# Optimization experiments

Measured on AMD Instinct MI355X. Metric: run time of the kernel, lower is better.

Reference implementation:

```python
import jax, jax.numpy as jnp
import numpy as np

T, B, I, H, L = 512, 128, 512, 512, 2


def setup_inputs() -> dict:
    key = jax.random.key(0)
    ks = jax.random.split(key, 9)
    s = 1.0 / np.sqrt(H)  # torch LSTM init: U(-1/sqrt(H), 1/sqrt(H))
    u = lambda k, shape: jax.random.uniform(k, shape, jnp.float32, -s, s)
    return {
        "input_seq": jax.random.normal(ks[0], (T, B, I), jnp.float32),
        "W_ih0": u(ks[1], (4 * H, I)),
        "W_hh0": u(ks[2], (4 * H, H)),
        "b_ih0": u(ks[3], (4 * H,)),
        "b_hh0": u(ks[4], (4 * H,)),
        "W_ih1": u(ks[5], (4 * H, H)),
        "W_hh1": u(ks[6], (4 * H, H)),
        "b_ih1": u(ks[7], (4 * H,)),
        "b_hh1": u(ks[8], (4 * H,)),
    }


def _lstm_layer(x, W_ih, W_hh, b_ih, b_hh):
    # x: (T, B, in). Gate order matches torch: i, f, g, o.
    Bv = x.shape[1]
    Hv = W_hh.shape[1]
    # Precompute input projections for all timesteps (one big GEMM).
    x_proj = jnp.einsum('tbi,gi->tbg', x, W_ih) + b_ih + b_hh  # (T,B,4H)

    def step(carry, xp):
        h, c = carry
        gates = xp + h @ W_hh.T  # (B,4H)
        i, f, g, o = jnp.split(gates, 4, axis=-1)
        c = jax.nn.sigmoid(f) * c + jax.nn.sigmoid(i) * jnp.tanh(g)
        h = jax.nn.sigmoid(o) * jnp.tanh(c)
        return (h, c), h

    h0 = jnp.zeros((Bv, Hv), x.dtype)
    _, hs = jax.lax.scan(step, (h0, h0), x_proj)
    return hs  # (T,B,H)


def reference(input_seq, W_ih0, W_hh0, b_ih0, b_hh0, W_ih1, W_hh1, b_ih1, b_hh1):
    h1 = _lstm_layer(input_seq, W_ih0, W_hh0, b_ih0, b_hh0)
    h2 = _lstm_layer(h1, W_ih1, W_hh1, b_ih1, b_hh1)
    return h2[-1]  # last timestep of top layer, (B,H)
```

## Files before the change

kernel.cpp:

```cpp
#include <hip/hip_runtime.h>

typedef _Float16 f16;
typedef _Float16 f16x8 __attribute__((ext_vector_type(8)));
typedef float    f32x16 __attribute__((ext_vector_type(16)));

#define T_STEPS 512
#define RING    16


__device__ __forceinline__ void gload_lds16(const void* g, void* l) {
  __builtin_amdgcn_global_load_lds((const __attribute__((address_space(1))) void*)g,
                                   (__attribute__((address_space(3))) void*)l,
                                   16, 0, 0);
}

__device__ __forceinline__ float sigm(float x) { return 1.0f / (1.0f + __expf(-x)); }
__device__ __forceinline__ float tanh_f(float x) { return 2.0f / (1.0f + __expf(-2.0f * x)) - 1.0f; }

__device__ __forceinline__ bool spin_until(int* p, int target) {
  int it = 0;
  while (__hip_atomic_load(p, __ATOMIC_RELAXED, __HIP_MEMORY_SCOPE_AGENT) < target) {
    __builtin_amdgcn_s_sleep(1);
    if (++it > (1 << 20)) return false;
  }
  return true;
}


__global__ void cvt_kernel(const float* __restrict__ in, f16* __restrict__ out, int n8) {
  int i = blockIdx.x * blockDim.x + threadIdx.x;
  if (i >= n8) return;
  const float4* p = (const float4*)in + (size_t)i * 2;
  float4 a = p[0], b = p[1];
  f16x8 v = {(f16)a.x, (f16)a.y, (f16)a.z, (f16)a.w,
             (f16)b.x, (f16)b.y, (f16)b.z, (f16)b.w};
  *((f16x8*)out + i) = v;
}


__launch_bounds__(256, 1)
__global__ void lstm_scan(const f16* __restrict__ X16,
                          f16* __restrict__ h1ring, f16* __restrict__ h2ring,
                          int* __restrict__ cnt1, int* __restrict__ cnt2,
                          const float* __restrict__ Wih0, const float* __restrict__ Whh0,
                          const float* __restrict__ bih0, const float* __restrict__ bhh0,
                          const float* __restrict__ Wih1, const float* __restrict__ Whh1,
                          const float* __restrict__ bih1, const float* __restrict__ bhh1,
                          float* __restrict__ out) {
  __shared__ __align__(16) char A_lds[65536];
  __shared__ float P[2][32][32];
  __shared__ float G[2][32][32];
  __shared__ float bias_lds[64];
  __shared__ float c_lds[512];

  const int bid  = blockIdx.x;
  const int xcd  = bid & 7;
  const int layer = xcd & 1;
  const int g    = xcd >> 1;
  const int j    = bid >> 3;
  const int tid  = threadIdx.x;
  const int w    = tid >> 6;
  const int lane = tid & 63;
  const int c32  = lane & 31;
  const int kgrp = lane >> 5;
  const int nt   = w & 1;
  const int kh   = w >> 1;

  const float* Wsrc = layer ? (kh ? Whh1 : Wih1) : (kh ? Whh0 : Wih0);
  const int q    = nt * 2 + (c32 >> 4);
  const int wcol = q * 512 + j * 16 + (c32 & 15);
  f16x8 wreg[32];
  {
    const float* wrow = Wsrc + (size_t)wcol * 512 + kgrp * 8;
#pragma unroll
    for (int s = 0; s < 32; ++s) {
      const float* p = wrow + s * 16;
      float4 a = *(const float4*)p;
      float4 b = *(const float4*)(p + 4);
      f16x8 v = {(f16)a.x, (f16)a.y, (f16)a.z, (f16)a.w,
                 (f16)b.x, (f16)b.y, (f16)b.z, (f16)b.w};
      wreg[s] = v;
    }
  }
  if (tid < 64) {
    int c = tid & 31, n = tid >> 5;
    int qq  = n * 2 + (c >> 4);
    int col = qq * 512 + j * 16 + (c & 15);
    bias_lds[tid] = layer ? (bih1[col] + bhh1[col]) : (bih0[col] + bhh0[col]);
  }
  for (int e = tid; e < 512; e += 256) c_lds[e] = 0.0f;
  __syncthreads();

  int* cntOwn = layer ? cnt2 : cnt1;
  const int b_stage = g * 32 + c32;

  bool alive = true;
  for (int t = 0; t < T_STEPS; ++t) {
    if (layer == 0 && w < 2) {
      const f16* base = X16 + (size_t)t * 65536;
      const f16* lsrc = base + (size_t)b_stage * 512 + nt * 256 + kgrp * 8;
      char* ldst = A_lds + w * 16384;
#pragma unroll
      for (int si = 0; si < 16; ++si) gload_lds16(lsrc + si * 16, ldst + si * 1024);
    }

    if (tid == 0) {
      if (alive) {
        if (layer == 0) {
          if (t > 0)     alive &= spin_until(&cnt1[(t - 1) * 4 + g], 32);
          if (t >= RING) alive &= spin_until(&cnt2[(t - RING) * 4 + g], 32);
        } else {
          alive &= spin_until(&cnt1[t * 4 + g], 32);
          if (t > 0) alive &= spin_until(&cnt2[(t - 1) * 4 + g], 32);
        }
      }
      __builtin_amdgcn_fence(__ATOMIC_ACQUIRE, "agent");
    }
    __syncthreads();

    {
      const f16* base = nullptr;
      if (layer == 0) {
        if (w >= 2) base = h1ring + (size_t)(t & (RING - 1)) * 65536;
      } else {
        base = (w < 2) ? (h1ring + (size_t)((t + 1) & (RING - 1)) * 65536)
                       : (h2ring + (size_t)(t & (RING - 1)) * 65536);
      }
      if (base) {
        const f16* lsrc = base + (size_t)b_stage * 512 + nt * 256 + kgrp * 8;
        char* ldst = A_lds + w * 16384;
#pragma unroll
        for (int si = 0; si < 16; ++si) gload_lds16(lsrc + si * 16, ldst + si * 1024);
      }
    }
    __syncthreads();

    f32x16 acc0 = {}, acc1 = {}, acc2 = {}, acc3 = {};
    {
      const char* afb = A_lds + kh * 32768 + kgrp * 512 + c32 * 16;
#pragma unroll
      for (int s = 0; s < 32; s += 4) {
        f16x8 a0 = *(const f16x8*)(afb + (size_t)(s + 0) * 1024);
        f16x8 a1 = *(const f16x8*)(afb + (size_t)(s + 1) * 1024);
        f16x8 a2 = *(const f16x8*)(afb + (size_t)(s + 2) * 1024);
        f16x8 a3 = *(const f16x8*)(afb + (size_t)(s + 3) * 1024);
        acc0 = __builtin_amdgcn_mfma_f32_32x32x16_f16(a0, wreg[s + 0], acc0, 0, 0, 0);
        acc1 = __builtin_amdgcn_mfma_f32_32x32x16_f16(a1, wreg[s + 1], acc1, 0, 0, 0);
        acc2 = __builtin_amdgcn_mfma_f32_32x32x16_f16(a2, wreg[s + 2], acc2, 0, 0, 0);
        acc3 = __builtin_amdgcn_mfma_f32_32x32x16_f16(a3, wreg[s + 3], acc3, 0, 0, 0);
      }
    }
    f32x16 accs = (acc0 + acc1) + (acc2 + acc3);

    if (kh == 1) {
#pragma unroll
      for (int i = 0; i < 16; ++i) {
        int row = (i & 3) + 8 * (i >> 2) + 4 * kgrp;
        P[nt][row][c32] = accs[i];
      }
    }
    __syncthreads();
    if (kh == 0) {
#pragma unroll
      for (int i = 0; i < 16; ++i) {
        int row = (i & 3) + 8 * (i >> 2) + 4 * kgrp;
        G[nt][row][c32] = accs[i] + P[nt][row][c32];
      }
    }
    __syncthreads();

    {
      f16* ring = layer ? h2ring : h1ring;
      const size_t slot = (size_t)((t + 1) & (RING - 1)) * 65536;
      const int e0 = tid * 2;
      const int r = e0 >> 4, cc = e0 & 15;
      float hv[2];
#pragma unroll
      for (int u = 0; u < 2; ++u) {
        int cu = cc + u;
        float iv = G[0][r][cu]      + bias_lds[cu];
        float fv = G[0][r][cu + 16] + bias_lds[cu + 16];
        float gv = G[1][r][cu]      + bias_lds[32 + cu];
        float ov = G[1][r][cu + 16] + bias_lds[48 + cu];
        float c  = sigm(fv) * c_lds[e0 + u] + sigm(iv) * tanh_f(gv);
        c_lds[e0 + u] = c;
        hv[u] = sigm(ov) * tanh_f(c);
      }
      union { f16 h2_[2]; int i32; } pk;
      pk.h2_[0] = (f16)hv[0]; pk.h2_[1] = (f16)hv[1];
      int* dst = (int*)(ring + slot + (size_t)(g * 32 + r) * 512 + (j * 16 + cc));
      __hip_atomic_store(dst, pk.i32, __ATOMIC_RELAXED, __HIP_MEMORY_SCOPE_AGENT);
      if (layer && t == T_STEPS - 1) {
        out[(size_t)(g * 32 + r) * 512 + (j * 16 + cc)]     = hv[0];
        out[(size_t)(g * 32 + r) * 512 + (j * 16 + cc) + 1] = hv[1];
      }
    }
    __syncthreads();

    if (tid == 0) {
      __hip_atomic_fetch_add(&cntOwn[t * 4 + g], 1,
                             __ATOMIC_RELAXED, __HIP_MEMORY_SCOPE_AGENT);
    }
  }
}


extern "C" void kernel_launch(void* const* d_in, const int* in_sizes, int n_in,
                              void* d_out, int out_size, void* d_ws, size_t ws_size,
                              hipStream_t stream) {
  const float* X    = (const float*)d_in[0];
  const float* Wih0 = (const float*)d_in[1];
  const float* Whh0 = (const float*)d_in[2];
  const float* bih0 = (const float*)d_in[3];
  const float* bhh0 = (const float*)d_in[4];
  const float* Wih1 = (const float*)d_in[5];
  const float* Whh1 = (const float*)d_in[6];
  const float* bih1 = (const float*)d_in[7];
  const float* bhh1 = (const float*)d_in[8];
  float* out = (float*)d_out;

  char* ws = (char*)d_ws;
  size_t off = 0;
  f16* X16 = (f16*)(ws + off); off += (size_t)512 * 128 * 512 * 2;
  f16* h1r = (f16*)(ws + off); off += (size_t)RING * 128 * 512 * 2;
  f16* h2r = (f16*)(ws + off); off += (size_t)RING * 128 * 512 * 2;
  int* cnt1 = (int*)(ws + off); off += (size_t)512 * 4 * 4;
  int* cnt2 = (int*)(ws + off); off += (size_t)512 * 4 * 4;
  if (ws_size < off) return;

  hipMemsetAsync(cnt1, 0, (size_t)512 * 4 * 4 * 2, stream);
  hipMemsetAsync(h1r, 0, (size_t)128 * 512 * 2, stream);
  hipMemsetAsync(h2r, 0, (size_t)128 * 512 * 2, stream);

  int n8 = (512 * 128 * 512) / 8;
  cvt_kernel<<<n8 / 256, 256, 0, stream>>>(X, X16, n8);
  lstm_scan<<<256, 256, 0, stream>>>(X16, h1r, h2r, cnt1, cnt2,
                                     Wih0, Whh0, bih0, bhh0,
                                     Wih1, Whh1, bih1, bhh1, out);
}
```

Measured before the change: 3.683 ms.

## Replace shared step counters with per-block flags and single-wave spin-then-load

Replaces per-timestep atomic counters with one monotonic flag per block, polled by a full wave with a ballot over the 32 producer blocks. The wave that waits then issues the recurrent-state LDS loads itself, removing a block barrier between the wait and the load. In layer 1 the h1 loads can start before the h2 wait completes. The two-stage partial-sum reduction is also collapsed into one LDS write plus a combined read, dropping another barrier. The trade-off is that one wave now issues all recurrent loads, so its load issue is serialized.

```diff
diff --git a/kernel.cpp b/kernel.cpp
--- a/kernel.cpp
+++ b/kernel.cpp
@@ -17,13 +17,15 @@
 __device__ __forceinline__ float sigm(float x) { return 1.0f / (1.0f + __expf(-x)); }
 __device__ __forceinline__ float tanh_f(float x) { return 2.0f / (1.0f + __expf(-2.0f * x)) - 1.0f; }
 
-__device__ __forceinline__ bool spin_until(int* p, int target) {
+__device__ __forceinline__ bool spin_flags(const int* f, int target) {
+  const int l = threadIdx.x & 31;
   int it = 0;
-  while (__hip_atomic_load(p, __ATOMIC_RELAXED, __HIP_MEMORY_SCOPE_AGENT) < target) {
+  while (true) {
+    int v = __hip_atomic_load(f + l, __ATOMIC_RELAXED, __HIP_MEMORY_SCOPE_AGENT);
+    if (__all(v >= target)) return true;
     __builtin_amdgcn_s_sleep(1);
     if (++it > (1 << 20)) return false;
   }
-  return true;
 }
 
 
@@ -41,15 +43,14 @@
 __launch_bounds__(256, 1)
 __global__ void lstm_scan(const f16* __restrict__ X16,
                           f16* __restrict__ h1ring, f16* __restrict__ h2ring,
-                          int* __restrict__ cnt1, int* __restrict__ cnt2,
+                          int* __restrict__ flags1, int* __restrict__ flags2,
                           const float* __restrict__ Wih0, const float* __restrict__ Whh0,
                           const float* __restrict__ bih0, const float* __restrict__ bhh0,
                           const float* __restrict__ Wih1, const float* __restrict__ Whh1,
                           const float* __restrict__ bih1, const float* __restrict__ bhh1,
                           float* __restrict__ out) {
   __shared__ __align__(16) char A_lds[65536];
-  __shared__ float P[2][32][32];
-  __shared__ float G[2][32][32];
+  __shared__ float P[2][2][32][33];
   __shared__ float bias_lds[64];
   __shared__ float c_lds[512];
 
@@ -91,46 +92,45 @@
   for (int e = tid; e < 512; e += 256) c_lds[e] = 0.0f;
   __syncthreads();
 
-  int* cntOwn = layer ? cnt2 : cnt1;
+  const int* f1g = flags1 + g * 32;
+  const int* f2g = flags2 + g * 32;
+  int* flagOwn = (layer ? flags2 : flags1) + g * 32 + j;
   const int b_stage = g * 32 + c32;
+  const int krow = b_stage * 512 + kgrp * 8;
 
   bool alive = true;
   for (int t = 0; t < T_STEPS; ++t) {
-    if (layer == 0 && w < 2) {
-      const f16* base = X16 + (size_t)t * 65536;
-      const f16* lsrc = base + (size_t)b_stage * 512 + nt * 256 + kgrp * 8;
-      char* ldst = A_lds + w * 16384;
-#pragma unroll
-      for (int si = 0; si < 16; ++si) gload_lds16(lsrc + si * 16, ldst + si * 1024);
-    }
-
-    if (tid == 0) {
-      if (alive) {
-        if (layer == 0) {
-          if (t > 0)     alive &= spin_until(&cnt1[(t - 1) * 4 + g], 32);
-          if (t >= RING) alive &= spin_until(&cnt2[(t - RING) * 4 + g], 32);
-        } else {
-          alive &= spin_until(&cnt1[t * 4 + g], 32);
-          if (t > 0) alive &= spin_until(&cnt2[(t - 1) * 4 + g], 32);
+    if (layer == 0) {
+      const f16* xb = X16 + (size_t)t * 65536 + krow + w * 128;
+      char* ld = A_lds + w * 8192;
+#pragma unroll
+      for (int si = 0; si < 8; ++si) gload_lds16(xb + si * 16, ld + si * 1024);
+    }
+
+    if (w == 0) {
+      if (layer == 0) {
+        if (alive) {
+          if (t > 0)     alive &= spin_flags(f1g, t);
+          if (t >= RING) alive &= spin_flags(f2g, t - RING + 1);
         }
-      }
-      __builtin_amdgcn_fence(__ATOMIC_ACQUIRE, "agent");
-    }
-    __syncthreads();
-
-    {
-      const f16* base = nullptr;
-      if (layer == 0) {
-        if (w >= 2) base = h1ring + (size_t)(t & (RING - 1)) * 65536;
+        __builtin_amdgcn_fence(__ATOMIC_ACQUIRE, "agent");
+        const f16* hb = h1ring + (size_t)(t & (RING - 1)) * 65536 + krow;
+#pragma unroll
+        for (int ks = 0; ks < 32; ++ks)
+          gload_lds16(hb + ks * 16, A_lds + (size_t)(32 + ks) * 1024);
       } else {
-        base = (w < 2) ? (h1ring + (size_t)((t + 1) & (RING - 1)) * 65536)
-                       : (h2ring + (size_t)(t & (RING - 1)) * 65536);
-      }
-      if (base) {
-        const f16* lsrc = base + (size_t)b_stage * 512 + nt * 256 + kgrp * 8;
-        char* ldst = A_lds + w * 16384;
-#pragma unroll
-        for (int si = 0; si < 16; ++si) gload_lds16(lsrc + si * 16, ldst + si * 1024);
+        if (alive) alive &= spin_flags(f1g, t + 1);
+        __builtin_amdgcn_fence(__ATOMIC_ACQUIRE, "agent");
+        const f16* h1b = h1ring + (size_t)((t + 1) & (RING - 1)) * 65536 + krow;
+#pragma unroll
+        for (int ks = 0; ks < 32; ++ks)
+          gload_lds16(h1b + ks * 16, A_lds + (size_t)ks * 1024);
+        if (alive && t > 0) alive &= spin_flags(f2g, t);
+        __builtin_amdgcn_fence(__ATOMIC_ACQUIRE, "agent");
+        const f16* h2b = h2ring + (size_t)(t & (RING - 1)) * 65536 + krow;
+#pragma unroll
+        for (int ks = 0; ks < 32; ++ks)
+          gload_lds16(h2b + ks * 16, A_lds + (size_t)(32 + ks) * 1024);
       }
     }
     __syncthreads();
@@ -152,20 +152,10 @@
     }
     f32x16 accs = (acc0 + acc1) + (acc2 + acc3);
 
-    if (kh == 1) {
-#pragma unroll
-      for (int i = 0; i < 16; ++i) {
-        int row = (i & 3) + 8 * (i >> 2) + 4 * kgrp;
-        P[nt][row][c32] = accs[i];
-      }
-    }
-    __syncthreads();
-    if (kh == 0) {
-#pragma unroll
-      for (int i = 0; i < 16; ++i) {
-        int row = (i & 3) + 8 * (i >> 2) + 4 * kgrp;
-        G[nt][row][c32] = accs[i] + P[nt][row][c32];
-      }
+#pragma unroll
+    for (int i = 0; i < 16; ++i) {
+      int row = (i & 3) + 8 * (i >> 2) + 4 * kgrp;
+      P[kh][nt][row][c32] = accs[i];
     }
     __syncthreads();
 
@@ -178,10 +168,10 @@
 #pragma unroll
       for (int u = 0; u < 2; ++u) {
         int cu = cc + u;
-        float iv = G[0][r][cu]      + bias_lds[cu];
-        float fv = G[0][r][cu + 16] + bias_lds[cu + 16];
-        float gv = G[1][r][cu]      + bias_lds[32 + cu];
-        float ov = G[1][r][cu + 16] + bias_lds[48 + cu];
+        float iv = P[0][0][r][cu]      + P[1][0][r][cu]      + bias_lds[cu];
+        float fv = P[0][0][r][cu + 16] + P[1][0][r][cu + 16] + bias_lds[cu + 16];
+        float gv = P[0][1][r][cu]      + P[1][1][r][cu]      + bias_lds[32 + cu];
+        float ov = P[0][1][r][cu + 16] + P[1][1][r][cu + 16] + bias_lds[48 + cu];
         float c  = sigm(fv) * c_lds[e0 + u] + sigm(iv) * tanh_f(gv);
         c_lds[e0 + u] = c;
         hv[u] = sigm(ov) * tanh_f(c);
@@ -197,10 +187,8 @@
     }
     __syncthreads();
 
-    if (tid == 0) {
-      __hip_atomic_fetch_add(&cntOwn[t * 4 + g], 1,
-                             __ATOMIC_RELAXED, __HIP_MEMORY_SCOPE_AGENT);
-    }
+    if (tid == 0)
+      __hip_atomic_store(flagOwn, t + 1, __ATOMIC_RELAXED, __HIP_MEMORY_SCOPE_AGENT);
   }
 }
 
@@ -224,17 +212,17 @@
   f16* X16 = (f16*)(ws + off); off += (size_t)512 * 128 * 512 * 2;
   f16* h1r = (f16*)(ws + off); off += (size_t)RING * 128 * 512 * 2;
   f16* h2r = (f16*)(ws + off); off += (size_t)RING * 128 * 512 * 2;
-  int* cnt1 = (int*)(ws + off); off += (size_t)512 * 4 * 4;
-  int* cnt2 = (int*)(ws + off); off += (size_t)512 * 4 * 4;
+  int* flags1 = (int*)(ws + off); off += 4 * 32 * 4;
+  int* flags2 = (int*)(ws + off); off += 4 * 32 * 4;
   if (ws_size < off) return;
 
-  hipMemsetAsync(cnt1, 0, (size_t)512 * 4 * 4 * 2, stream);
+  hipMemsetAsync(flags1, 0, 4 * 32 * 4 * 2, stream);
   hipMemsetAsync(h1r, 0, (size_t)128 * 512 * 2, stream);
   hipMemsetAsync(h2r, 0, (size_t)128 * 512 * 2, stream);
 
   int n8 = (512 * 128 * 512) / 8;
   cvt_kernel<<<n8 / 256, 256, 0, stream>>>(X, X16, n8);
-  lstm_scan<<<256, 256, 0, stream>>>(X16, h1r, h2r, cnt1, cnt2,
+  lstm_scan<<<256, 256, 0, stream>>>(X16, h1r, h2r, flags1, flags2,
                                      Wih0, Whh0, bih0, bhh0,
                                      Wih1, Whh1, bih1, bhh1, out);
 }
```

Result: faster. 3.415 ms (-7.3%).
